# Kernel optimization log

Measured on AMD Instinct MI355X. Metric: run time of the kernel, lower is better.

## Reference

```python
import jax, jax.numpy as jnp
import numpy as np

N_NODES = 50000
N_EDGES = 800000
IN_DIM = 128
HIDDEN = 32
HEADS = 4
OUT_DIM = 64
NEG_SLOPE = 0.2  # PyG GATConv default


def setup_inputs() -> dict:
    key = jax.random.key(0)
    ks = jax.random.split(key, 12)
    s = 0.05
    return {
        "x": jax.random.normal(ks[0], (N_NODES, IN_DIM), dtype=jnp.float32),
        "edge_index": jax.random.randint(ks[1], (2, N_EDGES), 0, N_NODES, dtype=jnp.int64),
        # layer 1: out = HEADS * HIDDEN, concat=True
        "W1": jax.random.normal(ks[2], (IN_DIM, HEADS * HIDDEN), dtype=jnp.float32) * s,
        "a_src1": jax.random.normal(ks[3], (HEADS, HIDDEN), dtype=jnp.float32) * s,
        "a_dst1": jax.random.normal(ks[4], (HEADS, HIDDEN), dtype=jnp.float32) * s,
        "b1": jnp.zeros((HEADS * HIDDEN,), dtype=jnp.float32),
        # layer 2: heads=1, concat=False
        "W2": jax.random.normal(ks[5], (HEADS * HIDDEN, OUT_DIM), dtype=jnp.float32) * s,
        "a_src2": jax.random.normal(ks[6], (1, OUT_DIM), dtype=jnp.float32) * s,
        "a_dst2": jax.random.normal(ks[7], (1, OUT_DIM), dtype=jnp.float32) * s,
        "b2": jnp.zeros((OUT_DIM,), dtype=jnp.float32),
    }


def _gat_conv(x, src, dst, W, a_src, a_dst, b, heads, concat):
    """PyG-style GATConv. src/dst already include self-loops."""
    N = x.shape[0]
    C = W.shape[1] // heads
    h = (x @ W).reshape(N, heads, C)              # [N,H,C]
    al_s = jnp.sum(h * a_src, axis=-1)            # [N,H]
    al_d = jnp.sum(h * a_dst, axis=-1)            # [N,H]
    e = jax.nn.leaky_relu(al_s[src] + al_d[dst], NEG_SLOPE)  # [E,H]
    # numerically-stable segment softmax over incoming edges of each dst node
    m = jax.ops.segment_max(e, dst, num_segments=N)          # [N,H]
    ex = jnp.exp(e - m[dst])
    denom = jax.ops.segment_sum(ex, dst, num_segments=N)     # [N,H]
    alpha = ex / denom[dst]                                   # [E,H]
    out = jax.ops.segment_sum(h[src] * alpha[:, :, None], dst, num_segments=N)  # [N,H,C]
    out = out.reshape(N, heads * C) if concat else out.mean(axis=1)
    return out + b


def reference(x, edge_index, W1, a_src1, a_dst1, b1, W2, a_src2, a_dst2, b2):
    N = x.shape[0]
    loop = jnp.arange(N, dtype=edge_index.dtype)
    src = jnp.concatenate([edge_index[0], loop])
    dst = jnp.concatenate([edge_index[1], loop])
    h = jax.nn.relu(_gat_conv(x, src, dst, W1, a_src1, a_dst1, b1, HEADS, True))
    out = _gat_conv(h, src, dst, W2, a_src2, a_dst2, b2, 1, False)
    return jax.nn.log_softmax(out, axis=1)
```

## Files before the change

### kernel.cpp

```cpp
#include <hip/hip_runtime.h>
#include <hip/hip_bf16.h>
#include <math.h>

#define N_NODES 50000
#define N_EDGES 800000
#define E_TOT   (N_EDGES + N_NODES)
#define IN_DIM  128
#define HID     128
#define ODIM    64
#define NEG     0.2f
#define NB1     ((N_NODES + 255) / 256)
#define NCHUNK  ((N_NODES + 31) / 32)
#define NREP    8

typedef short bf16x8 __attribute__((ext_vector_type(8)));
typedef float f32x4 __attribute__((ext_vector_type(4)));
typedef float f32x2 __attribute__((ext_vector_type(2)));
typedef unsigned short ushort_t;

__device__ __forceinline__ float lrelu(float x) { return x >= 0.f ? x : NEG * x; }

__device__ __forceinline__ unsigned short f2b(float v) {
  unsigned int b = __float_as_uint(v);
  b += 0x7fffu + ((b >> 16) & 1u);
  return (unsigned short)(b >> 16);
}
__device__ __forceinline__ float b2f(unsigned short u) {
  return __uint_as_float(((unsigned int)u) << 16);
}
__device__ __forceinline__ unsigned int f2b2(float lo, float hi) {
  union { __hip_bfloat162 h; unsigned int u; } cv;
  cv.h = __float22bfloat162_rn(make_float2(lo, hi));
  return cv.u;
}
__device__ __forceinline__ float blo(unsigned int v) { return __uint_as_float(v << 16); }
__device__ __forceinline__ float bhi(unsigned int v) { return __uint_as_float(v & 0xffff0000u); }

__device__ __forceinline__ f32x2 f8x2lo(unsigned int v) {
  return __builtin_amdgcn_cvt_pk_f32_fp8((int)v, false);
}
__device__ __forceinline__ f32x2 f8x2hi(unsigned int v) {
  return __builtin_amdgcn_cvt_pk_f32_fp8((int)v, true);
}
__device__ __forceinline__ unsigned char f2f8(float v) {
  return (unsigned char)(__builtin_amdgcn_cvt_pk_fp8_f32(v, v, 0, false) & 0xff);
}

__device__ __forceinline__ int e_src(const void* ei, int f, int e) {
  if (e >= N_EDGES) return e - N_EDGES;
  return f ? (int)((const long long*)ei)[e] : ((const int*)ei)[e];
}
__device__ __forceinline__ int e_dst(const void* ei, int f, int e) {
  if (e >= N_EDGES) return e - N_EDGES;
  return f ? (int)((const long long*)ei)[N_EDGES + e] : ((const int*)ei)[N_EDGES + e];
}

__global__ void k_prep(const float* __restrict__ W1, const float* __restrict__ W2,
                       ushort_t* __restrict__ Wt1, ushort_t* __restrict__ Wt2,
                       const void* ei, int* flag, int4* __restrict__ degr4) {
  if (blockIdx.x == 64) {
    if (threadIdx.x == 0) {
      const int* p = (const int*)ei;
      int allz = 1;
      for (int i = 0; i < 64; ++i) if (p[2 * i + 1] != 0) { allz = 0; break; }
      *flag = allz;
    }
    return;
  }
  if (blockIdx.x > 64) {
    int i = (blockIdx.x - 65) * 256 + threadIdx.x;
    if (i < NREP * N_NODES / 4) degr4[i] = make_int4(0, 0, 0, 0);
    return;
  }
  int i = blockIdx.x * 256 + threadIdx.x;
  if (i < 128 * 128) { int k = i >> 7, n = i & 127; Wt1[n * 128 + k] = f2b(W1[i]); }
  if (i < 128 * 64)  { int k = i >> 6, n = i & 63;  Wt2[n * 128 + k] = f2b(W2[i]); }
}

__global__ void k_hist(const void* ei, const int* flag, int* degr, int* rank) {
  int e = blockIdx.x * 256 + threadIdx.x;
  if (e >= E_TOT) return;
  int r = blockIdx.x & (NREP - 1);
  int d = e_dst(ei, *flag, e);
  rank[e] = atomicAdd(&degr[r * N_NODES + d], 1);
}

__global__ void k_scan1(const int* __restrict__ degr, int* __restrict__ offs, int* __restrict__ bsums) {
  __shared__ int sm[256];
  int t = threadIdx.x, i = blockIdx.x * 256 + t;
  int v = 0;
  if (i < N_NODES) {
    #pragma unroll
    for (int r = 0; r < NREP; ++r) v += degr[r * N_NODES + i];
  }
  sm[t] = v;
  __syncthreads();
  for (int o = 1; o < 256; o <<= 1) {
    int add = (t >= o) ? sm[t - o] : 0;
    __syncthreads();
    sm[t] += add;
    __syncthreads();
  }
  if (i < N_NODES) offs[i] = sm[t] - v;
  if (t == 255) bsums[blockIdx.x] = sm[255];
}

__global__ void k_scan3(int* __restrict__ offs, const int* __restrict__ bsums,
                        const int* __restrict__ degr, int* __restrict__ repbase) {
  __shared__ int red[4];
  int t = threadIdx.x;
  int v = (t < blockIdx.x) ? bsums[t] : 0;
  #pragma unroll
  for (int o = 32; o >= 1; o >>= 1) v += __shfl_xor(v, o);
  if ((t & 63) == 0) red[t >> 6] = v;
  __syncthreads();
  int pre = red[0] + red[1] + red[2] + red[3];
  int i = blockIdx.x * 256 + t;
  if (i < N_NODES) {
    int o = offs[i] + pre;
    offs[i] = o;
    int run = o;
    #pragma unroll
    for (int r = 0; r < NREP; ++r) {
      repbase[r * N_NODES + i] = run;
      run += degr[r * N_NODES + i];
    }
  }
  if (i == 0) offs[N_NODES] = E_TOT;
}

__global__ void k_scatter(const void* ei, const int* __restrict__ flag,
                          const int* __restrict__ repbase,
                          const int* __restrict__ rank, int* __restrict__ srcs) {
  int e = blockIdx.x * 256 + threadIdx.x;
  if (e >= E_TOT) return;
  int f = *flag;
  int d = e_dst(ei, f, e);
  int r = blockIdx.x & (NREP - 1);
  srcs[repbase[r * N_NODES + d] + rank[e]] = e_src(ei, f, e);
}

__global__ __launch_bounds__(256) void k_mm1(const float* __restrict__ x,
                                             const ushort_t* __restrict__ Wt,
                                             ushort_t* __restrict__ h1b,
                                             unsigned char* __restrict__ h1f8) {
  __shared__ ushort_t xs[32 * 128];
  int t = threadIdx.x;
  int w = t >> 6, l = t & 63;
  int lr = l & 15, lk = l >> 4;
  int nodeSub = (w & 1) * 16, colBase = (w >> 1) * 64;
  bf16x8 bfrag[4][4];
  #pragma unroll
  for (int ct = 0; ct < 4; ++ct)
    #pragma unroll
    for (int ks = 0; ks < 4; ++ks) {
      int n = colBase + ct * 16 + lr;
      int k = ks * 32 + lk * 8;
      bfrag[ct][ks] = *(const bf16x8*)&Wt[n * 128 + k];
    }
  int rr = t >> 3, c0 = (t & 7) * 16;
  for (int chunk = blockIdx.x; chunk < NCHUNK; chunk += gridDim.x) {
    int base = chunk * 32;
    int srcRow = base + rr; if (srcRow >= N_NODES) srcRow = N_NODES - 1;
    const float4* xr = (const float4*)&x[(size_t)srcRow * IN_DIM + c0];
    float4 f0 = xr[0], f1 = xr[1], f2 = xr[2], f3 = xr[3];
    uint4 w0, w1;
    w0.x = f2b2(f0.x, f0.y); w0.y = f2b2(f0.z, f0.w);
    w0.z = f2b2(f1.x, f1.y); w0.w = f2b2(f1.z, f1.w);
    w1.x = f2b2(f2.x, f2.y); w1.y = f2b2(f2.z, f2.w);
    w1.z = f2b2(f3.x, f3.y); w1.w = f2b2(f3.z, f3.w);
    char* xsb = (char*)xs;
    int swz = (rr & 7) << 4;
    *(uint4*)(xsb + rr * 256 + ((c0 * 2 +  0) ^ swz)) = w0;
    *(uint4*)(xsb + rr * 256 + ((c0 * 2 + 16) ^ swz)) = w1;
    __syncthreads();
    f32x4 acc[4] = {{0,0,0,0},{0,0,0,0},{0,0,0,0},{0,0,0,0}};
    int arow = nodeSub + lr;
    #pragma unroll
    for (int ks = 0; ks < 4; ++ks) {
      bf16x8 a = *(const bf16x8*)((const char*)xs + arow * 256 +
                                  ((ks * 64 + lk * 16) ^ ((arow & 7) << 4)));
      #pragma unroll
      for (int ct = 0; ct < 4; ++ct)
        acc[ct] = __builtin_amdgcn_mfma_f32_16x16x32_bf16(a, bfrag[ct][ks], acc[ct], 0, 0, 0);
    }
    __syncthreads();
    #pragma unroll
    for (int ct = 0; ct < 4; ++ct)
      #pragma unroll
      for (int r = 0; r < 4; ++r) {
        int node = base + nodeSub + lk * 4 + r;
        if (node < N_NODES) {
          float v = acc[ct][r];
          int col = colBase + ct * 16 + lr;
          h1b[(size_t)node * HID + col] = f2b(v);
          h1f8[(size_t)node * HID + col] = f2f8(v);
        }
      }
  }
}

__global__ __launch_bounds__(256) void k_mm2(const ushort_t* __restrict__ xb,
                                             const ushort_t* __restrict__ Wt,
                                             ushort_t* __restrict__ h2b,
                                             unsigned char* __restrict__ h2f8) {
  __shared__ ushort_t xs[32 * 128];
  int t = threadIdx.x;
  int w = t >> 6, l = t & 63;
  int lr = l & 15, lk = l >> 4;
  int nodeSub = (w & 1) * 16, colBase = (w >> 1) * 32;
  bf16x8 bfrag[2][4];
  #pragma unroll
  for (int ct = 0; ct < 2; ++ct)
    #pragma unroll
    for (int ks = 0; ks < 4; ++ks) {
      int n = colBase + ct * 16 + lr;
      int k = ks * 32 + lk * 8;
      bfrag[ct][ks] = *(const bf16x8*)&Wt[n * 128 + k];
    }
  int rr = t >> 3, c0 = (t & 7) * 16;
  for (int chunk = blockIdx.x; chunk < NCHUNK; chunk += gridDim.x) {
    int base = chunk * 32;
    int srcRow = base + rr; if (srcRow >= N_NODES) srcRow = N_NODES - 1;
    const uint4* xr = (const uint4*)&xb[(size_t)srcRow * HID + c0];
    uint4 w0 = xr[0], w1 = xr[1];
    char* xsb = (char*)xs;
    int swz = (rr & 7) << 4;
    *(uint4*)(xsb + rr * 256 + ((c0 * 2 +  0) ^ swz)) = w0;
    *(uint4*)(xsb + rr * 256 + ((c0 * 2 + 16) ^ swz)) = w1;
    __syncthreads();
    f32x4 acc[2] = {{0,0,0,0},{0,0,0,0}};
    int arow = nodeSub + lr;
    #pragma unroll
    for (int ks = 0; ks < 4; ++ks) {
      bf16x8 a = *(const bf16x8*)((const char*)xs + arow * 256 +
                                  ((ks * 64 + lk * 16) ^ ((arow & 7) << 4)));
      #pragma unroll
      for (int ct = 0; ct < 2; ++ct)
        acc[ct] = __builtin_amdgcn_mfma_f32_16x16x32_bf16(a, bfrag[ct][ks], acc[ct], 0, 0, 0);
    }
    __syncthreads();
    #pragma unroll
    for (int ct = 0; ct < 2; ++ct)
      #pragma unroll
      for (int r = 0; r < 4; ++r) {
        int node = base + nodeSub + lk * 4 + r;
        if (node < N_NODES) {
          float v = acc[ct][r];
          int col = colBase + ct * 16 + lr;
          h2b[(size_t)node * ODIM + col] = f2b(v);
          h2f8[(size_t)node * ODIM + col] = f2f8(v);
        }
      }
  }
}

__global__ __launch_bounds__(256) void k_al1(const ushort_t* __restrict__ h1b,
                                             const float* __restrict__ asrc,
                                             const float* __restrict__ adst, float* __restrict__ als,
                                             float* __restrict__ ald) {
  int t = threadIdx.x;
  int n = blockIdx.x * 16 + (t >> 4);
  int c8 = (t & 15) * 8;
  uint4 v = *(const uint4*)&h1b[(size_t)n * HID + c8];
  float4 a0 = *(const float4*)&asrc[c8], a1 = *(const float4*)&asrc[c8 + 4];
  float4 d0 = *(const float4*)&adst[c8], d1 = *(const float4*)&adst[c8 + 4];
  float f0 = blo(v.x), f1 = bhi(v.x), f2 = blo(v.y), f3 = bhi(v.y);
  float f4 = blo(v.z), f5 = bhi(v.z), f6 = blo(v.w), f7 = bhi(v.w);
  float s = f0*a0.x + f1*a0.y + f2*a0.z + f3*a0.w + f4*a1.x + f5*a1.y + f6*a1.z + f7*a1.w;
  float d = f0*d0.x + f1*d0.y + f2*d0.z + f3*d0.w + f4*d1.x + f5*d1.y + f6*d1.z + f7*d1.w;
  s += __shfl_xor(s, 1); s += __shfl_xor(s, 2);
  d += __shfl_xor(d, 1); d += __shfl_xor(d, 2);
  if ((t & 3) == 0) {
    int head = (t & 15) >> 2;
    als[n * 4 + head] = s;
    ald[n * 4 + head] = d;
  }
}

__global__ __launch_bounds__(256) void k_al2(const ushort_t* __restrict__ h2b,
                                             const float* __restrict__ asrc,
                                             const float* __restrict__ adst, float* __restrict__ als,
                                             float* __restrict__ ald) {
  int t = threadIdx.x;
  int n = blockIdx.x * 32 + (t >> 3);
  if (n >= N_NODES) return;
  int c8 = (t & 7) * 8;
  uint4 v = *(const uint4*)&h2b[(size_t)n * ODIM + c8];
  float4 a0 = *(const float4*)&asrc[c8], a1 = *(const float4*)&asrc[c8 + 4];
  float4 d0 = *(const float4*)&adst[c8], d1 = *(const float4*)&adst[c8 + 4];
  float f0 = blo(v.x), f1 = bhi(v.x), f2 = blo(v.y), f3 = bhi(v.y);
  float f4 = blo(v.z), f5 = bhi(v.z), f6 = blo(v.w), f7 = bhi(v.w);
  float s = f0*a0.x + f1*a0.y + f2*a0.z + f3*a0.w + f4*a1.x + f5*a1.y + f6*a1.z + f7*a1.w;
  float d = f0*d0.x + f1*d0.y + f2*d0.z + f3*d0.w + f4*d1.x + f5*d1.y + f6*d1.z + f7*d1.w;
  s += __shfl_xor(s, 1); s += __shfl_xor(s, 2); s += __shfl_xor(s, 4);
  d += __shfl_xor(d, 1); d += __shfl_xor(d, 2); d += __shfl_xor(d, 4);
  if ((t & 7) == 0) { als[n] = s; ald[n] = d; }
}

__global__ __launch_bounds__(256) void k_agg1(const unsigned char* __restrict__ h1f8,
                                              const float* __restrict__ als,
                                              const float* __restrict__ ald, const int* __restrict__ offs,
                                              const int* __restrict__ srcs, const float* __restrict__ b1,
                                              ushort_t* __restrict__ out1b) {
  int t = threadIdx.x;
  int w = t >> 6, l = t & 63;
  int hw = l >> 5, lh = l & 31;
  int sg = lh >> 4, cl = lh & 15, head = cl >> 2;
  int n = blockIdx.x * 8 + w * 2 + hw;
  int off0 = offs[n], deg = offs[n + 1] - off0;
  float adh = ald[n * 4 + head];
  const unsigned char* hb = h1f8 + cl * 8;

  float ds = 0.f;
  float num0 = 0, num1 = 0, num2 = 0, num3 = 0, num4 = 0, num5 = 0, num6 = 0, num7 = 0;

  int j = sg;
  for (; j + 2 < deg; j += 4) {
    int sA = srcs[off0 + j];
    int sB = srcs[off0 + j + 2];
    float aA = als[sA * 4 + head];
    float aB = als[sB * 4 + head];
    uint2 vA = *(const uint2*)(hb + (sA << 7));
    uint2 vB = *(const uint2*)(hb + (sB << 7));
    float wA = __expf(lrelu(aA + adh));
    float wB = __expf(lrelu(aB + adh));
    ds += wA + wB;
    f32x2 p0 = f8x2lo(vA.x), p1 = f8x2hi(vA.x);
    f32x2 p2 = f8x2lo(vA.y), p3 = f8x2hi(vA.y);
    num0 = fmaf(wA, p0.x, num0); num1 = fmaf(wA, p0.y, num1);
    num2 = fmaf(wA, p1.x, num2); num3 = fmaf(wA, p1.y, num3);
    num4 = fmaf(wA, p2.x, num4); num5 = fmaf(wA, p2.y, num5);
    num6 = fmaf(wA, p3.x, num6); num7 = fmaf(wA, p3.y, num7);
    p0 = f8x2lo(vB.x); p1 = f8x2hi(vB.x);
    p2 = f8x2lo(vB.y); p3 = f8x2hi(vB.y);
    num0 = fmaf(wB, p0.x, num0); num1 = fmaf(wB, p0.y, num1);
    num2 = fmaf(wB, p1.x, num2); num3 = fmaf(wB, p1.y, num3);
    num4 = fmaf(wB, p2.x, num4); num5 = fmaf(wB, p2.y, num5);
    num6 = fmaf(wB, p3.x, num6); num7 = fmaf(wB, p3.y, num7);
  }
  if (j < deg) {
    int sA = srcs[off0 + j];
    float aA = als[sA * 4 + head];
    uint2 vA = *(const uint2*)(hb + (sA << 7));
    float wA = __expf(lrelu(aA + adh));
    ds += wA;
    f32x2 p0 = f8x2lo(vA.x), p1 = f8x2hi(vA.x);
    f32x2 p2 = f8x2lo(vA.y), p3 = f8x2hi(vA.y);
    num0 = fmaf(wA, p0.x, num0); num1 = fmaf(wA, p0.y, num1);
    num2 = fmaf(wA, p1.x, num2); num3 = fmaf(wA, p1.y, num3);
    num4 = fmaf(wA, p2.x, num4); num5 = fmaf(wA, p2.y, num5);
    num6 = fmaf(wA, p3.x, num6); num7 = fmaf(wA, p3.y, num7);
  }
  num0 += __shfl_xor(num0, 16); num1 += __shfl_xor(num1, 16);
  num2 += __shfl_xor(num2, 16); num3 += __shfl_xor(num3, 16);
  num4 += __shfl_xor(num4, 16); num5 += __shfl_xor(num5, 16);
  num6 += __shfl_xor(num6, 16); num7 += __shfl_xor(num7, 16);
  ds += __shfl_xor(ds, 16);
  if (lh < 16) {
    float rd = 1.f / ds;
    int c8 = cl * 8;
    float4 bb0 = *(const float4*)&b1[c8];
    float4 bb1 = *(const float4*)&b1[c8 + 4];
    float o0 = fmaxf(num0 * rd + bb0.x, 0.f);
    float o1 = fmaxf(num1 * rd + bb0.y, 0.f);
    float o2 = fmaxf(num2 * rd + bb0.z, 0.f);
    float o3 = fmaxf(num3 * rd + bb0.w, 0.f);
    float o4 = fmaxf(num4 * rd + bb1.x, 0.f);
    float o5 = fmaxf(num5 * rd + bb1.y, 0.f);
    float o6 = fmaxf(num6 * rd + bb1.z, 0.f);
    float o7 = fmaxf(num7 * rd + bb1.w, 0.f);
    uint4 pk;
    pk.x = f2b2(o0, o1); pk.y = f2b2(o2, o3);
    pk.z = f2b2(o4, o5); pk.w = f2b2(o6, o7);
    *(uint4*)&out1b[(size_t)n * HID + c8] = pk;
  }
}

__global__ __launch_bounds__(256) void k_agg2(const unsigned char* __restrict__ h2f8,
                                              const float* __restrict__ als,
                                              const float* __restrict__ ald, const int* __restrict__ offs,
                                              const int* __restrict__ srcs, const float* __restrict__ b2,
                                              float* __restrict__ out) {
  int t = threadIdx.x;
  int w = t >> 6, l = t & 63;
  int hw = l >> 5, lh = l & 31;
  int sg = lh >> 3, cl = lh & 7;
  int n = blockIdx.x * 8 + w * 2 + hw;
  int off0 = offs[n], deg = offs[n + 1] - off0;
  float adv = ald[n];
  const unsigned char* hb = h2f8 + cl * 8;

  float ds = 0.f;
  float num0 = 0, num1 = 0, num2 = 0, num3 = 0, num4 = 0, num5 = 0, num6 = 0, num7 = 0;

  int j = sg;
  for (; j + 4 < deg; j += 8) {
    int sA = srcs[off0 + j];
    int sB = srcs[off0 + j + 4];
    float aA = als[sA];
    float aB = als[sB];
    uint2 vA = *(const uint2*)(hb + (sA << 6));
    uint2 vB = *(const uint2*)(hb + (sB << 6));
    float wA = __expf(lrelu(aA + adv));
    float wB = __expf(lrelu(aB + adv));
    ds += wA + wB;
    f32x2 p0 = f8x2lo(vA.x), p1 = f8x2hi(vA.x);
    f32x2 p2 = f8x2lo(vA.y), p3 = f8x2hi(vA.y);
    num0 = fmaf(wA, p0.x, num0); num1 = fmaf(wA, p0.y, num1);
    num2 = fmaf(wA, p1.x, num2); num3 = fmaf(wA, p1.y, num3);
    num4 = fmaf(wA, p2.x, num4); num5 = fmaf(wA, p2.y, num5);
    num6 = fmaf(wA, p3.x, num6); num7 = fmaf(wA, p3.y, num7);
    p0 = f8x2lo(vB.x); p1 = f8x2hi(vB.x);
    p2 = f8x2lo(vB.y); p3 = f8x2hi(vB.y);
    num0 = fmaf(wB, p0.x, num0); num1 = fmaf(wB, p0.y, num1);
    num2 = fmaf(wB, p1.x, num2); num3 = fmaf(wB, p1.y, num3);
    num4 = fmaf(wB, p2.x, num4); num5 = fmaf(wB, p2.y, num5);
    num6 = fmaf(wB, p3.x, num6); num7 = fmaf(wB, p3.y, num7);
  }
  if (j < deg) {
    int sA = srcs[off0 + j];
    float aA = als[sA];
    uint2 vA = *(const uint2*)(hb + (sA << 6));
    float wA = __expf(lrelu(aA + adv));
    ds += wA;
    f32x2 p0 = f8x2lo(vA.x), p1 = f8x2hi(vA.x);
    f32x2 p2 = f8x2lo(vA.y), p3 = f8x2hi(vA.y);
    num0 = fmaf(wA, p0.x, num0); num1 = fmaf(wA, p0.y, num1);
    num2 = fmaf(wA, p1.x, num2); num3 = fmaf(wA, p1.y, num3);
    num4 = fmaf(wA, p2.x, num4); num5 = fmaf(wA, p2.y, num5);
    num6 = fmaf(wA, p3.x, num6); num7 = fmaf(wA, p3.y, num7);
  }
  #pragma unroll
  for (int o = 8; o <= 16; o <<= 1) {
    num0 += __shfl_xor(num0, o); num1 += __shfl_xor(num1, o);
    num2 += __shfl_xor(num2, o); num3 += __shfl_xor(num3, o);
    num4 += __shfl_xor(num4, o); num5 += __shfl_xor(num5, o);
    num6 += __shfl_xor(num6, o); num7 += __shfl_xor(num7, o);
    ds += __shfl_xor(ds, o);
  }
  if (lh < 8) {
    float rd = 1.f / ds;
    int c8 = cl * 8;
    float4 bb0 = *(const float4*)&b2[c8];
    float4 bb1 = *(const float4*)&b2[c8 + 4];
    float v0 = num0 * rd + bb0.x, v1 = num1 * rd + bb0.y;
    float v2 = num2 * rd + bb0.z, v3 = num3 * rd + bb0.w;
    float v4 = num4 * rd + bb1.x, v5 = num5 * rd + bb1.y;
    float v6 = num6 * rd + bb1.z, v7 = num7 * rd + bb1.w;
    float mx = fmaxf(fmaxf(fmaxf(v0, v1), fmaxf(v2, v3)), fmaxf(fmaxf(v4, v5), fmaxf(v6, v7)));
    #pragma unroll
    for (int o = 1; o <= 4; o <<= 1) mx = fmaxf(mx, __shfl_xor(mx, o));
    float sum = __expf(v0 - mx) + __expf(v1 - mx) + __expf(v2 - mx) + __expf(v3 - mx)
              + __expf(v4 - mx) + __expf(v5 - mx) + __expf(v6 - mx) + __expf(v7 - mx);
    #pragma unroll
    for (int o = 1; o <= 4; o <<= 1) sum += __shfl_xor(sum, o);
    float ls = __logf(sum);
    float4 r0, r1;
    r0.x = (v0 - mx) - ls; r0.y = (v1 - mx) - ls; r0.z = (v2 - mx) - ls; r0.w = (v3 - mx) - ls;
    r1.x = (v4 - mx) - ls; r1.y = (v5 - mx) - ls; r1.z = (v6 - mx) - ls; r1.w = (v7 - mx) - ls;
    *(float4*)&out[(size_t)n * ODIM + c8] = r0;
    *(float4*)&out[(size_t)n * ODIM + c8 + 4] = r1;
  }
}

extern "C" void kernel_launch(void* const* d_in, const int* in_sizes, int n_in,
                              void* d_out, int out_size, void* d_ws, size_t ws_size,
                              hipStream_t stream) {
  const float* x   = (const float*)d_in[0];
  const void*  ei  = d_in[1];
  const float* W1  = (const float*)d_in[2];
  const float* as1 = (const float*)d_in[3];
  const float* ad1 = (const float*)d_in[4];
  const float* b1  = (const float*)d_in[5];
  const float* W2  = (const float*)d_in[6];
  const float* as2 = (const float*)d_in[7];
  const float* ad2 = (const float*)d_in[8];
  const float* b2  = (const float*)d_in[9];
  float* out = (float*)d_out;

  char* ws = (char*)d_ws;
  size_t o = 0;
  auto alloc = [&](size_t bytes) { void* p = (void*)(ws + o); o += (bytes + 255) & ~(size_t)255; return p; };
  ushort_t* h1b   = (ushort_t*)alloc((size_t)N_NODES * HID * 2);
  ushort_t* out1b = (ushort_t*)alloc((size_t)N_NODES * HID * 2);
  ushort_t* h2b   = (ushort_t*)alloc((size_t)N_NODES * ODIM * 2);
  unsigned char* h1f8 = (unsigned char*)alloc((size_t)N_NODES * HID);
  ushort_t* Wt1   = (ushort_t*)alloc((size_t)128 * 128 * 2);
  ushort_t* Wt2   = (ushort_t*)alloc((size_t)64 * 128 * 2);
  float* als1 = (float*)alloc((size_t)N_NODES * 4 * 4);
  float* ald1 = (float*)alloc((size_t)N_NODES * 4 * 4);
  float* als2 = (float*)alloc((size_t)N_NODES * 4);
  float* ald2 = (float*)alloc((size_t)N_NODES * 4);
  int*   degr = (int*)alloc((size_t)NREP * N_NODES * 4);
  int*   repbase = (int*)alloc((size_t)NREP * N_NODES * 4);
  int*   offs = (int*)alloc((size_t)(N_NODES + 1) * 4);
  int*   rank = (int*)alloc((size_t)E_TOT * 4);
  int*   srcs = (int*)alloc((size_t)E_TOT * 4);
  int*   bsums= (int*)alloc((size_t)NB1 * 4);
  int*   flag = (int*)alloc(4);
  unsigned char* h2f8 = (unsigned char*)rank;

  int prepGrid = 65 + (NREP * N_NODES / 4 + 255) / 256;
  k_prep   <<<prepGrid, 256, 0, stream>>>(W1, W2, Wt1, Wt2, ei, flag, (int4*)degr);

  int egrid = (E_TOT + 255) / 256;
  k_hist   <<<egrid, 256, 0, stream>>>(ei, flag, degr, rank);
  k_scan1  <<<NB1,   256, 0, stream>>>(degr, offs, bsums);
  k_scan3  <<<NB1,   256, 0, stream>>>(offs, bsums, degr, repbase);
  k_scatter<<<egrid, 256, 0, stream>>>(ei, flag, repbase, rank, srcs);

  k_mm1  <<<512, 256, 0, stream>>>(x, Wt1, h1b, h1f8);
  k_al1  <<<N_NODES / 16, 256, 0, stream>>>(h1b, as1, ad1, als1, ald1);
  k_agg1 <<<N_NODES / 8, 256, 0, stream>>>(h1f8, als1, ald1, offs, srcs, b1, out1b);

  k_mm2  <<<512, 256, 0, stream>>>(out1b, Wt2, h2b, h2f8);
  k_al2  <<<(N_NODES + 31) / 32, 256, 0, stream>>>(h2b, as2, ad2, als2, ald2);
  k_agg2 <<<N_NODES / 8, 256, 0, stream>>>(h2f8, als2, ald2, offs, srcs, b2, out);
}
```

Before: 133.3 us.

## Fuse attention logit dot-products into matmul epilogues and merge histogram into mm1

Computes the per-node attention logits (al_s, al_d) directly from the MFMA accumulators in k_mm1 and k_mm2 using shuffle reductions and LDS atomics. This removes the separate k_al1/k_al2 kernels and the bf16 copies of h1 and h2 that existed only to feed them. The degree histogram kernel is folded into extra blocks of the mm1 launch so the edge histogram runs alongside the matmul. Logits are now computed from fp32 accumulators instead of bf16-rounded values, which changes numerics slightly, and the combined launch mixes two very different workloads.

Result: faster. 120.0 us (median of 3 runs) (-10.0%).

```diff
diff --git a/kernel.cpp b/kernel.cpp
--- a/kernel.cpp
+++ b/kernel.cpp
@@ -12,6 +12,8 @@
 #define NB1     ((N_NODES + 255) / 256)
 #define NCHUNK  ((N_NODES + 31) / 32)
 #define NREP    8
+#define MM1B    512
+#define EGRID   ((E_TOT + 255) / 256)
 
 typedef short bf16x8 __attribute__((ext_vector_type(8)));
 typedef float f32x4 __attribute__((ext_vector_type(4)));
@@ -25,17 +27,11 @@
   b += 0x7fffu + ((b >> 16) & 1u);
   return (unsigned short)(b >> 16);
 }
-__device__ __forceinline__ float b2f(unsigned short u) {
-  return __uint_as_float(((unsigned int)u) << 16);
-}
 __device__ __forceinline__ unsigned int f2b2(float lo, float hi) {
   union { __hip_bfloat162 h; unsigned int u; } cv;
   cv.h = __float22bfloat162_rn(make_float2(lo, hi));
   return cv.u;
 }
-__device__ __forceinline__ float blo(unsigned int v) { return __uint_as_float(v << 16); }
-__device__ __forceinline__ float bhi(unsigned int v) { return __uint_as_float(v & 0xffff0000u); }
-
 __device__ __forceinline__ f32x2 f8x2lo(unsigned int v) {
   return __builtin_amdgcn_cvt_pk_f32_fp8((int)v, false);
 }
@@ -75,14 +71,6 @@
   int i = blockIdx.x * 256 + threadIdx.x;
   if (i < 128 * 128) { int k = i >> 7, n = i & 127; Wt1[n * 128 + k] = f2b(W1[i]); }
   if (i < 128 * 64)  { int k = i >> 6, n = i & 63;  Wt2[n * 128 + k] = f2b(W2[i]); }
-}
-
-__global__ void k_hist(const void* ei, const int* flag, int* degr, int* rank) {
-  int e = blockIdx.x * 256 + threadIdx.x;
-  if (e >= E_TOT) return;
-  int r = blockIdx.x & (NREP - 1);
-  int d = e_dst(ei, *flag, e);
-  rank[e] = atomicAdd(&degr[r * N_NODES + d], 1);
 }
 
 __global__ void k_scan1(const int* __restrict__ degr, int* __restrict__ offs, int* __restrict__ bsums) {
@@ -140,15 +128,30 @@
   srcs[repbase[r * N_NODES + d] + rank[e]] = e_src(ei, f, e);
 }
 
-__global__ __launch_bounds__(256) void k_mm1(const float* __restrict__ x,
-                                             const ushort_t* __restrict__ Wt,
-                                             ushort_t* __restrict__ h1b,
-                                             unsigned char* __restrict__ h1f8) {
+__global__ __launch_bounds__(256) void k_mm1h(const float* __restrict__ x,
+                                              const ushort_t* __restrict__ Wt,
+                                              unsigned char* __restrict__ h1f8,
+                                              float* __restrict__ als1,
+                                              float* __restrict__ ald1,
+                                              const float* __restrict__ asrc,
+                                              const float* __restrict__ adst,
+                                              const void* ei, const int* __restrict__ flag,
+                                              int* __restrict__ degr, int* __restrict__ rank) {
+  if (blockIdx.x >= MM1B) {
+    int e = (blockIdx.x - MM1B) * 256 + threadIdx.x;
+    if (e < E_TOT) {
+      int r = (blockIdx.x - MM1B) & (NREP - 1);
+      int d = e_dst(ei, *flag, e);
+      rank[e] = atomicAdd(&degr[r * N_NODES + d], 1);
+    }
+    return;
+  }
   __shared__ ushort_t xs[32 * 128];
   int t = threadIdx.x;
   int w = t >> 6, l = t & 63;
   int lr = l & 15, lk = l >> 4;
   int nodeSub = (w & 1) * 16, colBase = (w >> 1) * 64;
+  int headBase = colBase >> 5;
   bf16x8 bfrag[4][4];
   #pragma unroll
   for (int ct = 0; ct < 4; ++ct)
@@ -158,8 +161,12 @@
       int k = ks * 32 + lk * 8;
       bfrag[ct][ks] = *(const bf16x8*)&Wt[n * 128 + k];
     }
+  float as0 = asrc[colBase + lr],      as1v = asrc[colBase + 16 + lr];
+  float as2 = asrc[colBase + 32 + lr], as3 = asrc[colBase + 48 + lr];
+  float ad0 = adst[colBase + lr],      ad1v = adst[colBase + 16 + lr];
+  float ad2 = adst[colBase + 32 + lr], ad3 = adst[colBase + 48 + lr];
   int rr = t >> 3, c0 = (t & 7) * 16;
-  for (int chunk = blockIdx.x; chunk < NCHUNK; chunk += gridDim.x) {
+  for (int chunk = blockIdx.x; chunk < NCHUNK; chunk += MM1B) {
     int base = chunk * 32;
     int srcRow = base + rr; if (srcRow >= N_NODES) srcRow = N_NODES - 1;
     const float4* xr = (const float4*)&x[(size_t)srcRow * IN_DIM + c0];
@@ -186,25 +193,42 @@
     }
     __syncthreads();
     #pragma unroll
-    for (int ct = 0; ct < 4; ++ct)
+    for (int r = 0; r < 4; ++r) {
+      int node = base + nodeSub + lk * 4 + r;
+      if (node < N_NODES) {
+        h1f8[(size_t)node * HID + colBase +      lr] = f2f8(acc[0][r]);
+        h1f8[(size_t)node * HID + colBase + 16 + lr] = f2f8(acc[1][r]);
+        h1f8[(size_t)node * HID + colBase + 32 + lr] = f2f8(acc[2][r]);
+        h1f8[(size_t)node * HID + colBase + 48 + lr] = f2f8(acc[3][r]);
+      }
+      float s01 = acc[0][r] * as0 + acc[1][r] * as1v;
+      float s23 = acc[2][r] * as2 + acc[3][r] * as3;
+      float d01 = acc[0][r] * ad0 + acc[1][r] * ad1v;
+      float d23 = acc[2][r] * ad2 + acc[3][r] * ad3;
       #pragma unroll
-      for (int r = 0; r < 4; ++r) {
-        int node = base + nodeSub + lk * 4 + r;
-        if (node < N_NODES) {
-          float v = acc[ct][r];
-          int col = colBase + ct * 16 + lr;
-          h1b[(size_t)node * HID + col] = f2b(v);
-          h1f8[(size_t)node * HID + col] = f2f8(v);
-        }
+      for (int o = 1; o <= 8; o <<= 1) {
+        s01 += __shfl_xor(s01, o); s23 += __shfl_xor(s23, o);
+        d01 += __shfl_xor(d01, o); d23 += __shfl_xor(d23, o);
       }
+      if (lr == 0 && node < N_NODES) {
+        als1[node * 4 + headBase]     = s01;
+        als1[node * 4 + headBase + 1] = s23;
+        ald1[node * 4 + headBase]     = d01;
+        ald1[node * 4 + headBase + 1] = d23;
+      }
+    }
   }
 }
 
 __global__ __launch_bounds__(256) void k_mm2(const ushort_t* __restrict__ xb,
                                              const ushort_t* __restrict__ Wt,
-                                             ushort_t* __restrict__ h2b,
-                                             unsigned char* __restrict__ h2f8) {
+                                             unsigned char* __restrict__ h2f8,
+                                             float* __restrict__ als2,
+                                             float* __restrict__ ald2,
+                                             const float* __restrict__ asrc,
+                                             const float* __restrict__ adst) {
   __shared__ ushort_t xs[32 * 128];
+  __shared__ float als_lds[32], ald_lds[32];
   int t = threadIdx.x;
   int w = t >> 6, l = t & 63;
   int lr = l & 15, lk = l >> 4;
@@ -218,6 +242,8 @@
       int k = ks * 32 + lk * 8;
       bfrag[ct][ks] = *(const bf16x8*)&Wt[n * 128 + k];
     }
+  float as0 = asrc[colBase + lr], as1v = asrc[colBase + 16 + lr];
+  float ad0 = adst[colBase + lr], ad1v = adst[colBase + 16 + lr];
   int rr = t >> 3, c0 = (t & 7) * 16;
   for (int chunk = blockIdx.x; chunk < NCHUNK; chunk += gridDim.x) {
     int base = chunk * 32;
@@ -239,63 +265,34 @@
       for (int ct = 0; ct < 2; ++ct)
         acc[ct] = __builtin_amdgcn_mfma_f32_16x16x32_bf16(a, bfrag[ct][ks], acc[ct], 0, 0, 0);
     }
-    __syncthreads();
-    #pragma unroll
-    for (int ct = 0; ct < 2; ++ct)
+    if (t < 32) { als_lds[t] = 0.f; ald_lds[t] = 0.f; }
+    __syncthreads();
+    #pragma unroll
+    for (int r = 0; r < 4; ++r) {
+      int nodeLocal = nodeSub + lk * 4 + r;
+      int node = base + nodeLocal;
+      if (node < N_NODES) {
+        h2f8[(size_t)node * ODIM + colBase +      lr] = f2f8(acc[0][r]);
+        h2f8[(size_t)node * ODIM + colBase + 16 + lr] = f2f8(acc[1][r]);
+      }
+      float s = acc[0][r] * as0 + acc[1][r] * as1v;
+      float d = acc[0][r] * ad0 + acc[1][r] * ad1v;
       #pragma unroll
-      for (int r = 0; r < 4; ++r) {
-        int node = base + nodeSub + lk * 4 + r;
-        if (node < N_NODES) {
-          float v = acc[ct][r];
-          int col = colBase + ct * 16 + lr;
-          h2b[(size_t)node * ODIM + col] = f2b(v);
-          h2f8[(size_t)node * ODIM + col] = f2f8(v);
-        }
+      for (int o = 1; o <= 8; o <<= 1) {
+        s += __shfl_xor(s, o);
+        d += __shfl_xor(d, o);
       }
-  }
-}
-
-__global__ __launch_bounds__(256) void k_al1(const ushort_t* __restrict__ h1b,
-                                             const float* __restrict__ asrc,
-                                             const float* __restrict__ adst, float* __restrict__ als,
-                                             float* __restrict__ ald) {
-  int t = threadIdx.x;
-  int n = blockIdx.x * 16 + (t >> 4);
-  int c8 = (t & 15) * 8;
-  uint4 v = *(const uint4*)&h1b[(size_t)n * HID + c8];
-  float4 a0 = *(const float4*)&asrc[c8], a1 = *(const float4*)&asrc[c8 + 4];
-  float4 d0 = *(const float4*)&adst[c8], d1 = *(const float4*)&adst[c8 + 4];
-  float f0 = blo(v.x), f1 = bhi(v.x), f2 = blo(v.y), f3 = bhi(v.y);
-  float f4 = blo(v.z), f5 = bhi(v.z), f6 = blo(v.w), f7 = bhi(v.w);
-  float s = f0*a0.x + f1*a0.y + f2*a0.z + f3*a0.w + f4*a1.x + f5*a1.y + f6*a1.z + f7*a1.w;
-  float d = f0*d0.x + f1*d0.y + f2*d0.z + f3*d0.w + f4*d1.x + f5*d1.y + f6*d1.z + f7*d1.w;
-  s += __shfl_xor(s, 1); s += __shfl_xor(s, 2);
-  d += __shfl_xor(d, 1); d += __shfl_xor(d, 2);
-  if ((t & 3) == 0) {
-    int head = (t & 15) >> 2;
-    als[n * 4 + head] = s;
-    ald[n * 4 + head] = d;
-  }
-}
-
-__global__ __launch_bounds__(256) void k_al2(const ushort_t* __restrict__ h2b,
-                                             const float* __restrict__ asrc,
-                                             const float* __restrict__ adst, float* __restrict__ als,
-                                             float* __restrict__ ald) {
-  int t = threadIdx.x;
-  int n = blockIdx.x * 32 + (t >> 3);
-  if (n >= N_NODES) return;
-  int c8 = (t & 7) * 8;
-  uint4 v = *(const uint4*)&h2b[(size_t)n * ODIM + c8];
-  float4 a0 = *(const float4*)&asrc[c8], a1 = *(const float4*)&asrc[c8 + 4];
-  float4 d0 = *(const float4*)&adst[c8], d1 = *(const float4*)&adst[c8 + 4];
-  float f0 = blo(v.x), f1 = bhi(v.x), f2 = blo(v.y), f3 = bhi(v.y);
-  float f4 = blo(v.z), f5 = bhi(v.z), f6 = blo(v.w), f7 = bhi(v.w);
-  float s = f0*a0.x + f1*a0.y + f2*a0.z + f3*a0.w + f4*a1.x + f5*a1.y + f6*a1.z + f7*a1.w;
-  float d = f0*d0.x + f1*d0.y + f2*d0.z + f3*d0.w + f4*d1.x + f5*d1.y + f6*d1.z + f7*d1.w;
-  s += __shfl_xor(s, 1); s += __shfl_xor(s, 2); s += __shfl_xor(s, 4);
-  d += __shfl_xor(d, 1); d += __shfl_xor(d, 2); d += __shfl_xor(d, 4);
-  if ((t & 7) == 0) { als[n] = s; ald[n] = d; }
+      if (lr == 0) {
+        atomicAdd(&als_lds[nodeLocal], s);
+        atomicAdd(&ald_lds[nodeLocal], d);
+      }
+    }
+    __syncthreads();
+    if (t < 32) {
+      int node = base + t;
+      if (node < N_NODES) { als2[node] = als_lds[t]; ald2[node] = ald_lds[t]; }
+    }
+  }
 }
 
 __global__ __launch_bounds__(256) void k_agg1(const unsigned char* __restrict__ h1f8,
@@ -482,9 +479,7 @@
   char* ws = (char*)d_ws;
   size_t o = 0;
   auto alloc = [&](size_t bytes) { void* p = (void*)(ws + o); o += (bytes + 255) & ~(size_t)255; return p; };
-  ushort_t* h1b   = (ushort_t*)alloc((size_t)N_NODES * HID * 2);
   ushort_t* out1b = (ushort_t*)alloc((size_t)N_NODES * HID * 2);
-  ushort_t* h2b   = (ushort_t*)alloc((size_t)N_NODES * ODIM * 2);
   unsigned char* h1f8 = (unsigned char*)alloc((size_t)N_NODES * HID);
   ushort_t* Wt1   = (ushort_t*)alloc((size_t)128 * 128 * 2);
   ushort_t* Wt2   = (ushort_t*)alloc((size_t)64 * 128 * 2);
@@ -504,17 +499,14 @@
   int prepGrid = 65 + (NREP * N_NODES / 4 + 255) / 256;
   k_prep   <<<prepGrid, 256, 0, stream>>>(W1, W2, Wt1, Wt2, ei, flag, (int4*)degr);
 
-  int egrid = (E_TOT + 255) / 256;
-  k_hist   <<<egrid, 256, 0, stream>>>(ei, flag, degr, rank);
-  k_scan1  <<<NB1,   256, 0, stream>>>(degr, offs, bsums);
-  k_scan3  <<<NB1,   256, 0, stream>>>(offs, bsums, degr, repbase);
-  k_scatter<<<egrid, 256, 0, stream>>>(ei, flag, repbase, rank, srcs);
-
-  k_mm1  <<<512, 256, 0, stream>>>(x, Wt1, h1b, h1f8);
-  k_al1  <<<N_NODES / 16, 256, 0, stream>>>(h1b, as1, ad1, als1, ald1);
+  k_mm1h   <<<MM1B + EGRID, 256, 0, stream>>>(x, Wt1, h1f8, als1, ald1, as1, ad1,
+                                              ei, flag, degr, rank);
+  k_scan1  <<<NB1, 256, 0, stream>>>(degr, offs, bsums);
+  k_scan3  <<<NB1, 256, 0, stream>>>(offs, bsums, degr, repbase);
+  k_scatter<<<EGRID, 256, 0, stream>>>(ei, flag, repbase, rank, srcs);
+
   k_agg1 <<<N_NODES / 8, 256, 0, stream>>>(h1f8, als1, ald1, offs, srcs, b1, out1b);
 
-  k_mm2  <<<512, 256, 0, stream>>>(out1b, Wt2, h2b, h2f8);
-  k_al2  <<<(N_NODES + 31) / 32, 256, 0, stream>>>(h2b, as2, ad2, als2, ald2);
+  k_mm2  <<<512, 256, 0, stream>>>(out1b, Wt2, h2f8, als2, ald2, as2, ad2);
   k_agg2 <<<N_NODES / 8, 256, 0, stream>>>(h2f8, als2, ald2, offs, srcs, b2, out);
 }
```
